# Performance work log

Measured on AMD Instinct MI355X. Metric: run time of the kernel, lower is better.

Reference implementation:

```python
import jax, jax.numpy as jnp
import numpy as np

N_CAM, N_PTS, N_OBS = 2000, 500000, 5000000


def setup_inputs() -> dict:
    key = jax.random.key(0)
    k1, k2, k3, k4, k5, k6 = jax.random.split(key, 6)
    # SE3 poses: [tx, ty, tz, qx, qy, qz, qw] (pypose layout), unit quaternions
    t = jax.random.normal(k1, (N_CAM, 3), dtype=jnp.float32) * 5.0
    t = t.at[:, 2].set(jax.random.uniform(k2, (N_CAM,), minval=100.0, maxval=200.0))
    q = jax.random.normal(k3, (N_CAM, 4), dtype=jnp.float32)
    q = q / jnp.linalg.norm(q, axis=-1, keepdims=True)
    poses = jnp.concatenate([t, q], axis=-1)  # [N_CAM, 7]
    points = jax.random.normal(k4, (N_PTS, 3), dtype=jnp.float32) * 5.0  # [N_PTS, 3]
    # Pinhole intrinsics
    K = jnp.array([[1000.0, 0.0, 640.0], [0.0, 1000.0, 360.0], [0.0, 0.0, 1.0]], dtype=jnp.float32)
    observes = jax.random.normal(k5, (N_OBS, 2), dtype=jnp.float32) * 100.0 + 500.0
    ki, kj = jax.random.split(k6)
    cidx = jax.random.randint(ki, (N_OBS,), 0, N_CAM, dtype=jnp.int64)
    pidx = jax.random.randint(kj, (N_OBS,), 0, N_PTS, dtype=jnp.int64)
    return {"observes": observes, "K": K, "poses": poses, "points": points, "cidx": cidx, "pidx": pidx}


def _se3_act(pose7, pts):
    # pose7: [N,7] (t, q) with q=(x,y,z,w); pts: [N,3]
    t = pose7[:, :3]
    qv = pose7[:, 3:6]
    qw = pose7[:, 6:7]
    # p' = p + 2 * qv x (qv x p + w p) + t   (unit-quaternion rotation)
    uv = jnp.cross(qv, pts)
    return pts + 2.0 * jnp.cross(qv, uv + qw * pts) + t


def reference(observes, K, poses, points, cidx, pidx):
    p_cam = _se3_act(poses[cidx], points[pidx])  # [N_OBS, 3] camera-frame points
    img = p_cam @ K.T                            # [N_OBS, 3] homogeneous pixels
    projs = img[:, :2] / img[:, 2:3]             # [N_OBS, 2]
    return (projs - observes).reshape(-1)        # [N_OBS * 2]
```

## Files before the change

kernel.cpp:

```cpp
#include <hip/hip_runtime.h>


typedef float    vfloat4 __attribute__((ext_vector_type(4)));
typedef int      vint4   __attribute__((ext_vector_type(4)));
typedef _Float16 vhalf4  __attribute__((ext_vector_type(4)));
typedef _Float16 vhalf8  __attribute__((ext_vector_type(8)));

#define MAX_CAM 2000

__global__ __launch_bounds__(256) void pack_points_h(
    const float* __restrict__ src, vhalf4* __restrict__ dst, int n_pts)
{
    int i = blockIdx.x * blockDim.x + threadIdx.x;
    if (i >= n_pts) return;
    const float* s = src + 3 * i;
    vhalf4 v = {(_Float16)s[0], (_Float16)s[1], (_Float16)s[2], (_Float16)0.0f};
    dst[i] = v;
}

__global__ __launch_bounds__(256) void pack_poses_h(
    const float* __restrict__ src, vhalf8* __restrict__ dst, int n_cam)
{
    int i = blockIdx.x * blockDim.x + threadIdx.x;
    if (i >= n_cam) return;
    const float* s = src + 7 * i;
    vhalf8 v = {(_Float16)s[0], (_Float16)s[1], (_Float16)s[2],
                (_Float16)s[3], (_Float16)s[4], (_Float16)s[5],
                (_Float16)s[6], (_Float16)0.0f};
    dst[i] = v;
}

__global__ __launch_bounds__(512) void resid_pipe(
    const float*  __restrict__ obs,
    const float*  __restrict__ Kmat,
    const vhalf8* __restrict__ poses_h,
    const vhalf4* __restrict__ points_h,
    const int*    __restrict__ cidx,
    const int*    __restrict__ pidx,
    float*        __restrict__ out,
    int n, int n_cam)
{
    __shared__ vhalf8 sposes[MAX_CAM];

    for (int r = threadIdx.x; r < n_cam; r += blockDim.x)
        sposes[r] = poses_h[r];
    __syncthreads();

    float fx = Kmat[0], cx = Kmat[2];
    float fy = Kmat[4], cy = Kmat[5];

    int nchunk = n >> 2;
    int tot    = gridDim.x * blockDim.x;
    int i      = blockIdx.x * blockDim.x + threadIdx.x;

    vint4 c_cur = {0, 0, 0, 0}, p_cur = {0, 0, 0, 0};
    if (i < nchunk) {
        c_cur = __builtin_nontemporal_load((const vint4*)(cidx + 4 * i));
        p_cur = __builtin_nontemporal_load((const vint4*)(pidx + 4 * i));
    }

    while (i < nchunk) {
        int base  = 4 * i;
        int inext = i + tot;

        vhalf4 P0 = points_h[p_cur.x];
        vhalf4 P1 = points_h[p_cur.y];
        vhalf4 P2 = points_h[p_cur.z];
        vhalf4 P3 = points_h[p_cur.w];

        vfloat4 o01 = __builtin_nontemporal_load((const vfloat4*)(obs + 2 * base));
        vfloat4 o23 = __builtin_nontemporal_load((const vfloat4*)(obs + 2 * base + 4));

        vint4 c_nxt = c_cur, p_nxt = p_cur;
        if (inext < nchunk) {
            c_nxt = __builtin_nontemporal_load((const vint4*)(cidx + 4 * inext));
            p_nxt = __builtin_nontemporal_load((const vint4*)(pidx + 4 * inext));
        }

        vhalf8 Q0 = sposes[c_cur.x];
        vhalf8 Q1 = sposes[c_cur.y];
        vhalf8 Q2 = sposes[c_cur.z];
        vhalf8 Q3 = sposes[c_cur.w];

        vhalf4 P[4]  = {P0, P1, P2, P3};
        vhalf8 Q[4]  = {Q0, Q1, Q2, Q3};
        float res[8];
        #pragma unroll
        for (int k = 0; k < 4; ++k) {
            float px = (float)P[k].x, py = (float)P[k].y, pz = (float)P[k].z;
            float tx = (float)Q[k][0], ty = (float)Q[k][1], tz = (float)Q[k][2];
            float qx = (float)Q[k][3], qy = (float)Q[k][4],
                  qz = (float)Q[k][5], qw = (float)Q[k][6];

            float ux = qy * pz - qz * py;
            float uy = qz * px - qx * pz;
            float uz = qx * py - qy * px;
            float wx = ux + qw * px;
            float wy = uy + qw * py;
            float wz = uz + qw * pz;
            float ccx = qy * wz - qz * wy;
            float ccy = qz * wx - qx * wz;
            float ccz = qx * wy - qy * wx;
            float X = px + 2.0f * ccx + tx;
            float Y = py + 2.0f * ccy + ty;
            float Z = pz + 2.0f * ccz + tz;

            float invz = 1.0f / Z;
            res[2 * k]     = fx * X * invz + cx;
            res[2 * k + 1] = fy * Y * invz + cy;
        }

        vfloat4 r0 = {res[0] - o01.x, res[1] - o01.y, res[2] - o01.z, res[3] - o01.w};
        vfloat4 r1 = {res[4] - o23.x, res[5] - o23.y, res[6] - o23.z, res[7] - o23.w};
        __builtin_nontemporal_store(r0, (vfloat4*)(out + 2 * base));
        __builtin_nontemporal_store(r1, (vfloat4*)(out + 2 * base + 4));

        i = inext;
        c_cur = c_nxt;
        p_cur = p_nxt;
    }

    if (blockIdx.x == 0 && threadIdx.x == 0) {
        for (int j = nchunk * 4; j < n; ++j) {
            vhalf4 P = points_h[pidx[j]];
            vhalf8 Q = sposes[cidx[j]];
            float px = (float)P.x, py = (float)P.y, pz = (float)P.z;
            float tx = (float)Q[0], ty = (float)Q[1], tz = (float)Q[2];
            float qx = (float)Q[3], qy = (float)Q[4], qz = (float)Q[5], qw = (float)Q[6];

            float ux = qy * pz - qz * py;
            float uy = qz * px - qx * pz;
            float uz = qx * py - qy * px;
            float wx = ux + qw * px;
            float wy = uy + qw * py;
            float wz = uz + qw * pz;
            float ccx = qy * wz - qz * wy;
            float ccy = qz * wx - qx * wz;
            float ccz = qx * wy - qy * wx;
            float X = px + 2.0f * ccx + tx;
            float Y = py + 2.0f * ccy + ty;
            float Z = pz + 2.0f * ccz + tz;

            float invz = 1.0f / Z;
            out[2 * j]     = fx * X * invz + cx - obs[2 * j];
            out[2 * j + 1] = fy * Y * invz + cy - obs[2 * j + 1];
        }
    }
}

__global__ __launch_bounds__(256) void resid_fallback(
    const float* __restrict__ obs, const float* __restrict__ Kmat,
    const float* __restrict__ poses, const float* __restrict__ points,
    const int* __restrict__ cidx, const int* __restrict__ pidx,
    float* __restrict__ out, int n)
{
    int i = blockIdx.x * blockDim.x + threadIdx.x;
    if (i >= n) return;
    const float* ps = poses + 7 * cidx[i];
    const float* pt = points + 3 * pidx[i];
    float px = pt[0], py = pt[1], pz = pt[2];
    float tx = ps[0], ty = ps[1], tz = ps[2];
    float qx = ps[3], qy = ps[4], qz = ps[5], qw = ps[6];
    float ux = qy * pz - qz * py;
    float uy = qz * px - qx * pz;
    float uz = qx * py - qy * px;
    float wx = ux + qw * px;
    float wy = uy + qw * py;
    float wz = uz + qw * pz;
    float ccx = qy * wz - qz * wy;
    float ccy = qz * wx - qx * wz;
    float ccz = qx * wy - qy * wx;
    float X = px + 2.0f * ccx + tx;
    float Y = py + 2.0f * ccy + ty;
    float Z = pz + 2.0f * ccz + tz;
    float invz = 1.0f / Z;
    out[2 * i]     = Kmat[0] * X * invz + Kmat[2] - obs[2 * i];
    out[2 * i + 1] = Kmat[4] * Y * invz + Kmat[5] - obs[2 * i + 1];
}

extern "C" void kernel_launch(void* const* d_in, const int* in_sizes, int n_in,
                              void* d_out, int out_size, void* d_ws, size_t ws_size,
                              hipStream_t stream) {
    const float* obs    = (const float*)d_in[0];
    const float* Kmat   = (const float*)d_in[1];
    const float* poses  = (const float*)d_in[2];
    const float* points = (const float*)d_in[3];
    const int*   cidx   = (const int*)d_in[4];
    const int*   pidx   = (const int*)d_in[5];
    float*       out    = (float*)d_out;

    int n     = in_sizes[4];
    int n_cam = in_sizes[2] / 7;
    int n_pts = in_sizes[3] / 3;

    size_t pts_bytes  = (size_t)n_pts * sizeof(vhalf4);
    size_t pose_bytes = (size_t)n_cam * sizeof(vhalf8);

    if (ws_size < pts_bytes + pose_bytes || n_cam > MAX_CAM) {
        resid_fallback<<<(n + 255) / 256, 256, 0, stream>>>(
            obs, Kmat, poses, points, cidx, pidx, out, n);
        return;
    }

    vhalf4* points_h = (vhalf4*)d_ws;
    vhalf8* poses_h  = (vhalf8*)((char*)d_ws + pts_bytes);

    pack_points_h<<<(n_pts + 255) / 256, 256, 0, stream>>>(points, points_h, n_pts);
    pack_poses_h<<<(n_cam + 255) / 256, 256, 0, stream>>>(poses, poses_h, n_cam);

    int block = 512;
    int grid  = 1024;
    resid_pipe<<<grid, block, 0, stream>>>(
        obs, Kmat, poses_h, points_h, cidx, pidx, out, n, n_cam);
}
```

Before: 163.1 us.

## Fuse pose packing into main kernel and balance contiguous wave-blocks per wave

Drops the separate pose-packing kernel launch; each block now converts the fp32 poses to fp16 directly while filling its shared-memory table. The grid-stride loop is replaced by a static per-wave partition of contiguous 64-chunk blocks, which balances work across waves and gives each wave a contiguous range of indices and observations. A leftover partial wave-block is handled by block 0's first wave. The trade-off is that every one of the 1024 blocks re-reads and converts the strided fp32 pose array, instead of copying a prepacked fp16 table.

```diff
diff --git a/kernel.cpp b/kernel.cpp
--- a/kernel.cpp
+++ b/kernel.cpp
@@ -18,22 +18,37 @@
     dst[i] = v;
 }
 
-__global__ __launch_bounds__(256) void pack_poses_h(
-    const float* __restrict__ src, vhalf8* __restrict__ dst, int n_cam)
-{
-    int i = blockIdx.x * blockDim.x + threadIdx.x;
-    if (i >= n_cam) return;
-    const float* s = src + 7 * i;
-    vhalf8 v = {(_Float16)s[0], (_Float16)s[1], (_Float16)s[2],
-                (_Float16)s[3], (_Float16)s[4], (_Float16)s[5],
-                (_Float16)s[6], (_Float16)0.0f};
-    dst[i] = v;
-}
-
-__global__ __launch_bounds__(512) void resid_pipe(
+__device__ __forceinline__ void project1(
+    vhalf4 P, vhalf8 Q, float fx, float fy, float cx, float cy,
+    float* rx, float* ry)
+{
+    float px = (float)P.x, py = (float)P.y, pz = (float)P.z;
+    float tx = (float)Q[0], ty = (float)Q[1], tz = (float)Q[2];
+    float qx = (float)Q[3], qy = (float)Q[4],
+          qz = (float)Q[5], qw = (float)Q[6];
+
+    float ux = qy * pz - qz * py;
+    float uy = qz * px - qx * pz;
+    float uz = qx * py - qy * px;
+    float wx = ux + qw * px;
+    float wy = uy + qw * py;
+    float wz = uz + qw * pz;
+    float ccx = qy * wz - qz * wy;
+    float ccy = qz * wx - qx * wz;
+    float ccz = qx * wy - qy * wx;
+    float X = px + 2.0f * ccx + tx;
+    float Y = py + 2.0f * ccy + ty;
+    float Z = pz + 2.0f * ccz + tz;
+
+    float invz = 1.0f / Z;
+    *rx = fx * X * invz + cx;
+    *ry = fy * Y * invz + cy;
+}
+
+__global__ __launch_bounds__(512) void resid_bal(
     const float*  __restrict__ obs,
     const float*  __restrict__ Kmat,
-    const vhalf8* __restrict__ poses_h,
+    const float*  __restrict__ poses,
     const vhalf4* __restrict__ points_h,
     const int*    __restrict__ cidx,
     const int*    __restrict__ pidx,
@@ -42,108 +57,106 @@
 {
     __shared__ vhalf8 sposes[MAX_CAM];
 
-    for (int r = threadIdx.x; r < n_cam; r += blockDim.x)
-        sposes[r] = poses_h[r];
+    for (int r = threadIdx.x; r < n_cam; r += blockDim.x) {
+        const float* s = poses + 7 * r;
+        vhalf8 v = {(_Float16)s[0], (_Float16)s[1], (_Float16)s[2],
+                    (_Float16)s[3], (_Float16)s[4], (_Float16)s[5],
+                    (_Float16)s[6], (_Float16)0.0f};
+        sposes[r] = v;
+    }
     __syncthreads();
 
     float fx = Kmat[0], cx = Kmat[2];
     float fy = Kmat[4], cy = Kmat[5];
 
     int nchunk = n >> 2;
-    int tot    = gridDim.x * blockDim.x;
-    int i      = blockIdx.x * blockDim.x + threadIdx.x;
-
-    vint4 c_cur = {0, 0, 0, 0}, p_cur = {0, 0, 0, 0};
-    if (i < nchunk) {
-        c_cur = __builtin_nontemporal_load((const vint4*)(cidx + 4 * i));
-        p_cur = __builtin_nontemporal_load((const vint4*)(pidx + 4 * i));
-    }
-
-    while (i < nchunk) {
-        int base  = 4 * i;
-        int inext = i + tot;
-
-        vhalf4 P0 = points_h[p_cur.x];
-        vhalf4 P1 = points_h[p_cur.y];
-        vhalf4 P2 = points_h[p_cur.z];
-        vhalf4 P3 = points_h[p_cur.w];
-
-        vfloat4 o01 = __builtin_nontemporal_load((const vfloat4*)(obs + 2 * base));
-        vfloat4 o23 = __builtin_nontemporal_load((const vfloat4*)(obs + 2 * base + 4));
-
-        vint4 c_nxt = c_cur, p_nxt = p_cur;
-        if (inext < nchunk) {
-            c_nxt = __builtin_nontemporal_load((const vint4*)(cidx + 4 * inext));
-            p_nxt = __builtin_nontemporal_load((const vint4*)(pidx + 4 * inext));
+    int nwb    = nchunk >> 6;
+    int lane   = threadIdx.x & 63;
+    int wave   = (blockIdx.x * blockDim.x + threadIdx.x) >> 6;
+    int nwave  = (gridDim.x * blockDim.x) >> 6;
+
+    int wb  = (int)(((long long)wave       * nwb) / nwave);
+    int wbe = (int)(((long long)(wave + 1) * nwb) / nwave);
+
+    if (wb < wbe) {
+        int i0 = (wb << 6) + lane;
+        vint4 c_cur = __builtin_nontemporal_load((const vint4*)(cidx + 4 * i0));
+        vint4 p_cur = __builtin_nontemporal_load((const vint4*)(pidx + 4 * i0));
+
+        while (wb < wbe) {
+            int i    = (wb << 6) + lane;
+            int base = 4 * i;
+
+            vhalf4 P0 = points_h[p_cur.x];
+            vhalf4 P1 = points_h[p_cur.y];
+            vhalf4 P2 = points_h[p_cur.z];
+            vhalf4 P3 = points_h[p_cur.w];
+
+            vfloat4 o01 = __builtin_nontemporal_load((const vfloat4*)(obs + 2 * base));
+            vfloat4 o23 = __builtin_nontemporal_load((const vfloat4*)(obs + 2 * base + 4));
+
+            int wbn = wb + 1;
+            vint4 c_nxt = c_cur, p_nxt = p_cur;
+            if (wbn < wbe) {
+                int inext = (wbn << 6) + lane;
+                c_nxt = __builtin_nontemporal_load((const vint4*)(cidx + 4 * inext));
+                p_nxt = __builtin_nontemporal_load((const vint4*)(pidx + 4 * inext));
+            }
+
+            vhalf8 Q0 = sposes[c_cur.x];
+            vhalf8 Q1 = sposes[c_cur.y];
+            vhalf8 Q2 = sposes[c_cur.z];
+            vhalf8 Q3 = sposes[c_cur.w];
+
+            vhalf4 P[4] = {P0, P1, P2, P3};
+            vhalf8 Q[4] = {Q0, Q1, Q2, Q3};
+            float res[8];
+            #pragma unroll
+            for (int k = 0; k < 4; ++k)
+                project1(P[k], Q[k], fx, fy, cx, cy, &res[2 * k], &res[2 * k + 1]);
+
+            vfloat4 r0 = {res[0] - o01.x, res[1] - o01.y, res[2] - o01.z, res[3] - o01.w};
+            vfloat4 r1 = {res[4] - o23.x, res[5] - o23.y, res[6] - o23.z, res[7] - o23.w};
+            __builtin_nontemporal_store(r0, (vfloat4*)(out + 2 * base));
+            __builtin_nontemporal_store(r1, (vfloat4*)(out + 2 * base + 4));
+
+            wb = wbn;
+            c_cur = c_nxt;
+            p_cur = p_nxt;
         }
-
-        vhalf8 Q0 = sposes[c_cur.x];
-        vhalf8 Q1 = sposes[c_cur.y];
-        vhalf8 Q2 = sposes[c_cur.z];
-        vhalf8 Q3 = sposes[c_cur.w];
-
-        vhalf4 P[4]  = {P0, P1, P2, P3};
-        vhalf8 Q[4]  = {Q0, Q1, Q2, Q3};
-        float res[8];
-        #pragma unroll
-        for (int k = 0; k < 4; ++k) {
-            float px = (float)P[k].x, py = (float)P[k].y, pz = (float)P[k].z;
-            float tx = (float)Q[k][0], ty = (float)Q[k][1], tz = (float)Q[k][2];
-            float qx = (float)Q[k][3], qy = (float)Q[k][4],
-                  qz = (float)Q[k][5], qw = (float)Q[k][6];
-
-            float ux = qy * pz - qz * py;
-            float uy = qz * px - qx * pz;
-            float uz = qx * py - qy * px;
-            float wx = ux + qw * px;
-            float wy = uy + qw * py;
-            float wz = uz + qw * pz;
-            float ccx = qy * wz - qz * wy;
-            float ccy = qz * wx - qx * wz;
-            float ccz = qx * wy - qy * wx;
-            float X = px + 2.0f * ccx + tx;
-            float Y = py + 2.0f * ccy + ty;
-            float Z = pz + 2.0f * ccz + tz;
-
-            float invz = 1.0f / Z;
-            res[2 * k]     = fx * X * invz + cx;
-            res[2 * k + 1] = fy * Y * invz + cy;
+    }
+
+    if (blockIdx.x == 0 && threadIdx.x < 64) {
+        int i = (nwb << 6) + lane;
+        if (i < nchunk) {
+            int base = 4 * i;
+            vint4 c_cur = *(const vint4*)(cidx + 4 * i);
+            vint4 p_cur = *(const vint4*)(pidx + 4 * i);
+            vhalf4 P[4] = {points_h[p_cur.x], points_h[p_cur.y],
+                           points_h[p_cur.z], points_h[p_cur.w]};
+            vhalf8 Q[4] = {sposes[c_cur.x], sposes[c_cur.y],
+                           sposes[c_cur.z], sposes[c_cur.w]};
+            vfloat4 o01 = *(const vfloat4*)(obs + 2 * base);
+            vfloat4 o23 = *(const vfloat4*)(obs + 2 * base + 4);
+            float res[8];
+            #pragma unroll
+            for (int k = 0; k < 4; ++k)
+                project1(P[k], Q[k], fx, fy, cx, cy, &res[2 * k], &res[2 * k + 1]);
+            vfloat4 r0 = {res[0] - o01.x, res[1] - o01.y, res[2] - o01.z, res[3] - o01.w};
+            vfloat4 r1 = {res[4] - o23.x, res[5] - o23.y, res[6] - o23.z, res[7] - o23.w};
+            *(vfloat4*)(out + 2 * base)     = r0;
+            *(vfloat4*)(out + 2 * base + 4) = r1;
         }
-
-        vfloat4 r0 = {res[0] - o01.x, res[1] - o01.y, res[2] - o01.z, res[3] - o01.w};
-        vfloat4 r1 = {res[4] - o23.x, res[5] - o23.y, res[6] - o23.z, res[7] - o23.w};
-        __builtin_nontemporal_store(r0, (vfloat4*)(out + 2 * base));
-        __builtin_nontemporal_store(r1, (vfloat4*)(out + 2 * base + 4));
-
-        i = inext;
-        c_cur = c_nxt;
-        p_cur = p_nxt;
     }
 
     if (blockIdx.x == 0 && threadIdx.x == 0) {
-        for (int j = nchunk * 4; j < n; ++j) {
+        for (int j = (nchunk << 2); j < n; ++j) {
             vhalf4 P = points_h[pidx[j]];
             vhalf8 Q = sposes[cidx[j]];
-            float px = (float)P.x, py = (float)P.y, pz = (float)P.z;
-            float tx = (float)Q[0], ty = (float)Q[1], tz = (float)Q[2];
-            float qx = (float)Q[3], qy = (float)Q[4], qz = (float)Q[5], qw = (float)Q[6];
-
-            float ux = qy * pz - qz * py;
-            float uy = qz * px - qx * pz;
-            float uz = qx * py - qy * px;
-            float wx = ux + qw * px;
-            float wy = uy + qw * py;
-            float wz = uz + qw * pz;
-            float ccx = qy * wz - qz * wy;
-            float ccy = qz * wx - qx * wz;
-            float ccz = qx * wy - qy * wx;
-            float X = px + 2.0f * ccx + tx;
-            float Y = py + 2.0f * ccy + ty;
-            float Z = pz + 2.0f * ccz + tz;
-
-            float invz = 1.0f / Z;
-            out[2 * j]     = fx * X * invz + cx - obs[2 * j];
-            out[2 * j + 1] = fy * Y * invz + cy - obs[2 * j + 1];
+            float rx, ry;
+            project1(P, Q, fx, fy, cx, cy, &rx, &ry);
+            out[2 * j]     = rx - obs[2 * j];
+            out[2 * j + 1] = ry - obs[2 * j + 1];
         }
     }
 }
@@ -193,23 +206,20 @@
     int n_cam = in_sizes[2] / 7;
     int n_pts = in_sizes[3] / 3;
 
-    size_t pts_bytes  = (size_t)n_pts * sizeof(vhalf4);
-    size_t pose_bytes = (size_t)n_cam * sizeof(vhalf8);
-
-    if (ws_size < pts_bytes + pose_bytes || n_cam > MAX_CAM) {
+    size_t pts_bytes = (size_t)n_pts * sizeof(vhalf4);
+
+    if (ws_size < pts_bytes || n_cam > MAX_CAM) {
         resid_fallback<<<(n + 255) / 256, 256, 0, stream>>>(
             obs, Kmat, poses, points, cidx, pidx, out, n);
         return;
     }
 
     vhalf4* points_h = (vhalf4*)d_ws;
-    vhalf8* poses_h  = (vhalf8*)((char*)d_ws + pts_bytes);
 
     pack_points_h<<<(n_pts + 255) / 256, 256, 0, stream>>>(points, points_h, n_pts);
-    pack_poses_h<<<(n_cam + 255) / 256, 256, 0, stream>>>(poses, poses_h, n_cam);
 
     int block = 512;
     int grid  = 1024;
-    resid_pipe<<<grid, block, 0, stream>>>(
-        obs, Kmat, poses_h, points_h, cidx, pidx, out, n, n_cam);
-}
+    resid_bal<<<grid, block, 0, stream>>>(
+        obs, Kmat, poses, points_h, cidx, pidx, out, n, n_cam);
+}
```

Measured after the change: 161.7 us. No clear change (-0.9%).
